# Performance work log

Hardware: AMD Instinct MI355X
Metric: run time of the kernel (lower is better)

Reference implementation:

```python
import jax, jax.numpy as jnp
import numpy as np

N_NODES = 100000
N_EDGES = 3200000
D_FEAT = 128
HIDDEN = 16
N_CLASSES = 8


def setup_inputs() -> dict:
    key = jax.random.key(0)
    k1, k2, k3, k4 = jax.random.split(key, 4)
    x = jax.random.normal(k1, (N_NODES, D_FEAT), dtype=jnp.float32)
    edge_index = jax.random.randint(k2, (2, N_EDGES), 0, N_NODES, dtype=jnp.int64)
    W1 = jax.random.normal(k3, (D_FEAT, HIDDEN), dtype=jnp.float32) * (1.0 / np.sqrt(D_FEAT))
    b1 = jnp.zeros((HIDDEN,), dtype=jnp.float32)
    W2 = jax.random.normal(k4, (HIDDEN, N_CLASSES), dtype=jnp.float32) * (1.0 / np.sqrt(HIDDEN))
    b2 = jnp.zeros((N_CLASSES,), dtype=jnp.float32)
    return {"x": x, "edge_index": edge_index, "W1": W1, "b1": b1, "W2": W2, "b2": b2}


def _gcn_conv(x, W, b, src, dst, deg_inv_sqrt, n_nodes):
    h = x @ W  # [N, F_out]
    norm = deg_inv_sqrt[src] * deg_inv_sqrt[dst]  # [E']
    msg = h[src] * norm[:, None]  # gather + scale
    out = jax.ops.segment_sum(msg, dst, num_segments=n_nodes)  # scatter-add
    return out + b


def _prep_edges(edge_index, n_nodes):
    # add self-loops (PyG GCNConv default) and compute symmetric norm degrees
    loop = jnp.arange(n_nodes, dtype=edge_index.dtype)
    src = jnp.concatenate([edge_index[0], loop])
    dst = jnp.concatenate([edge_index[1], loop])
    deg = jax.ops.segment_sum(jnp.ones_like(dst, dtype=jnp.float32), dst,
                              num_segments=n_nodes)
    deg_inv_sqrt = jnp.where(deg > 0, jax.lax.rsqrt(jnp.maximum(deg, 1.0)), 0.0)
    return src, dst, deg_inv_sqrt


def reference(x, edge_index, W1, b1, W2, b2):
    n_nodes = x.shape[0]
    src, dst, deg_inv_sqrt = _prep_edges(edge_index, n_nodes)
    h = jax.nn.relu(_gcn_conv(x, W1, b1, src, dst, deg_inv_sqrt, n_nodes))
    logits = _gcn_conv(h, W2, b2, src, dst, deg_inv_sqrt, n_nodes)
    return jax.nn.log_softmax(logits, axis=1)
```

## Files before the change

kernel.cpp:

```cpp
#include <hip/hip_runtime.h>

#define N_NODES 100000
#define N_EDGES 3200000
#define D_FEAT 128
#define HIDDEN 16
#define NCLS 8
#define NB_SCAN ((N_NODES + 255) / 256)


__global__ void k_deg_init(unsigned* __restrict__ deg) {
    int i = blockIdx.x * blockDim.x + threadIdx.x;
    if (i < N_NODES) deg[i] = 0u;
}

__global__ void k_deg_count(const int* __restrict__ dst, unsigned* __restrict__ deg) {
    int i = blockIdx.x * blockDim.x + threadIdx.x;
    if (i < N_EDGES) atomicAdd(&deg[dst[i]], 1u);
}

__global__ void k_dis(const unsigned* __restrict__ deg, float* __restrict__ dis) {
    int i = blockIdx.x * blockDim.x + threadIdx.x;
    if (i < N_NODES) dis[i] = rsqrtf((float)(deg[i] + 1u));
}

__global__ void k_scan1(const unsigned* __restrict__ deg, unsigned* __restrict__ rp,
                        unsigned* __restrict__ bsum) {
    __shared__ unsigned s[256];
    int tid = threadIdx.x;
    int i = blockIdx.x * 256 + tid;
    unsigned v = (i < N_NODES) ? deg[i] : 0u;
    s[tid] = v; __syncthreads();
    for (int off = 1; off < 256; off <<= 1) {
        unsigned t = (tid >= off) ? s[tid - off] : 0u;
        __syncthreads();
        s[tid] += t;
        __syncthreads();
    }
    if (i < N_NODES) rp[i] = s[tid] - v;
    if (tid == 255) bsum[blockIdx.x] = s[255];
}

__global__ void k_scan2(unsigned* __restrict__ bsum) {
    __shared__ unsigned s[512];
    int tid = threadIdx.x;
    unsigned v = (tid < NB_SCAN) ? bsum[tid] : 0u;
    s[tid] = v; __syncthreads();
    for (int off = 1; off < 512; off <<= 1) {
        unsigned t = (tid >= off) ? s[tid - off] : 0u;
        __syncthreads();
        s[tid] += t;
        __syncthreads();
    }
    bsum[tid] = s[tid] - v;
}

__global__ void k_scan3(unsigned* __restrict__ rp, const unsigned* __restrict__ bsum) {
    int i = blockIdx.x * blockDim.x + threadIdx.x;
    if (i < N_NODES) rp[i] += bsum[i >> 8];
}

__global__ void k_csr_fill(const int* __restrict__ src, const int* __restrict__ dst,
                           unsigned* __restrict__ rp, unsigned* __restrict__ csr) {
    int e = blockIdx.x * blockDim.x + threadIdx.x;
    if (e < N_EDGES) {
        unsigned p = atomicAdd(&rp[dst[e]], 1u);
        csr[p] = (unsigned)src[e];
    }
}

__global__ __launch_bounds__(256) void k_gemm1(const float* __restrict__ x,
                                               const float* __restrict__ W1,
                                               const float* __restrict__ dis,
                                               float* __restrict__ hd1) {
    __shared__ float sW[D_FEAT * HIDDEN];
    __shared__ float sx[64][132];
    int tid = threadIdx.x;
    for (int t = tid; t < D_FEAT * HIDDEN; t += 256) sW[t] = W1[t];

    int node0 = blockIdx.x * 64;
    #pragma unroll
    for (int it = 0; it < 8; ++it) {
        int lin = it * 256 + tid;
        int r   = lin >> 5;
        int c4  = lin & 31;
        int row = node0 + r;
        float4 v = make_float4(0.f, 0.f, 0.f, 0.f);
        if (row < N_NODES)
            v = *(const float4*)(x + (size_t)row * D_FEAT + c4 * 4);
        *(float4*)(&sx[r][c4 * 4]) = v;
    }
    __syncthreads();

    int lr   = tid >> 2;
    int node = node0 + lr;
    int f0   = (tid & 3) * 4;
    if (node >= N_NODES) return;

    float a0 = 0.f, a1 = 0.f, a2 = 0.f, a3 = 0.f;
    #pragma unroll
    for (int k = 0; k < D_FEAT; ++k) {
        float xv = sx[lr][k];
        a0 += xv * sW[k * HIDDEN + f0 + 0];
        a1 += xv * sW[k * HIDDEN + f0 + 1];
        a2 += xv * sW[k * HIDDEN + f0 + 2];
        a3 += xv * sW[k * HIDDEN + f0 + 3];
    }
    float s = dis[node];
    *(float4*)(hd1 + (size_t)node * HIDDEN + f0) = make_float4(a0 * s, a1 * s, a2 * s, a3 * s);
}

__global__ __launch_bounds__(256) void k_gather16_l2(
        const unsigned* __restrict__ rp, const unsigned* __restrict__ csr,
        const float* __restrict__ hd1, const float* __restrict__ dis,
        const float* __restrict__ b1, const float* __restrict__ W2,
        float* __restrict__ hd2) {
    __shared__ float sh[16][17];
    __shared__ float sW2[HIDDEN * NCLS];
    __shared__ float sb1[HIDDEN];
    int tid = threadIdx.x;
    if (tid < HIDDEN * NCLS) sW2[tid] = W2[tid];
    if (tid < HIDDEN)        sb1[tid] = b1[tid];

    int n = tid >> 4;
    int j = tid & 15;
    int node = blockIdx.x * 16 + n;

    unsigned start = (node == 0) ? 0u : rp[node - 1];
    unsigned end   = rp[node];
    float acc = hd1[(size_t)node * HIDDEN + j];
    for (unsigned e = start; e < end; ++e) {
        unsigned s = csr[e];
        acc += hd1[(size_t)s * HIDDEN + j];
    }
    float dv = dis[node];
    __syncthreads();
    float h = fmaxf(dv * acc + sb1[j], 0.f);
    sh[n][j] = h;
    __syncthreads();
    if (j < NCLS) {
        float o = 0.f;
        #pragma unroll
        for (int m = 0; m < HIDDEN; ++m) o += sh[n][m] * sW2[m * NCLS + j];
        hd2[(size_t)node * NCLS + j] = dv * o;
    }
}

__global__ __launch_bounds__(256) void k_gather8_final(
        const unsigned* __restrict__ rp, const unsigned* __restrict__ csr,
        const float* __restrict__ hd2, const float* __restrict__ dis,
        const float* __restrict__ b2, float* __restrict__ out) {
    int tid = threadIdx.x;
    int node = blockIdx.x * 32 + (tid >> 3);
    int j = tid & 7;

    unsigned start = (node == 0) ? 0u : rp[node - 1];
    unsigned end   = rp[node];
    float acc = hd2[(size_t)node * NCLS + j];
    for (unsigned e = start; e < end; ++e)
        acc += hd2[(size_t)csr[e] * NCLS + j];

    float l = dis[node] * acc + b2[j];
    float m = l;
    m = fmaxf(m, __shfl_xor(m, 1, 8));
    m = fmaxf(m, __shfl_xor(m, 2, 8));
    m = fmaxf(m, __shfl_xor(m, 4, 8));
    float ex = __expf(l - m);
    float ssum = ex;
    ssum += __shfl_xor(ssum, 1, 8);
    ssum += __shfl_xor(ssum, 2, 8);
    ssum += __shfl_xor(ssum, 4, 8);
    out[(size_t)node * NCLS + j] = l - (logf(ssum) + m);
}

extern "C" void kernel_launch(void* const* d_in, const int* in_sizes, int n_in,
                              void* d_out, int out_size, void* d_ws, size_t ws_size,
                              hipStream_t stream) {
    const float* x  = (const float*)d_in[0];
    const int*   ei = (const int*)d_in[1];
    const float* W1 = (const float*)d_in[2];
    const float* b1 = (const float*)d_in[3];
    const float* W2 = (const float*)d_in[4];
    const float* b2 = (const float*)d_in[5];
    float* out = (float*)d_out;

    const int* src = ei;
    const int* dst = ei + N_EDGES;

    unsigned* ws = (unsigned*)d_ws;
    const size_t N = N_NODES;
    unsigned* deg  = ws;
    float*    dis  = (float*)(ws + N);
    unsigned* rp   = ws + 2 * N;
    unsigned* bsum = ws + 3 * N;
    unsigned* csr  = ws + 3 * N + 512;
    float*    hd1  = (float*)(ws + 3 * N + 512 + N_EDGES);
    float*    hd2  = hd1 + 16 * N;

    const int TB = 256;
    int nb_nodes = (N_NODES + TB - 1) / TB;
    int nb_edges = (N_EDGES + TB - 1) / TB;

    k_deg_init<<<nb_nodes, TB, 0, stream>>>(deg);
    k_deg_count<<<nb_edges, TB, 0, stream>>>(dst, deg);
    k_dis<<<nb_nodes, TB, 0, stream>>>(deg, dis);

    k_scan1<<<NB_SCAN, 256, 0, stream>>>(deg, rp, bsum);
    k_scan2<<<1, 512, 0, stream>>>(bsum);
    k_scan3<<<nb_nodes, TB, 0, stream>>>(rp, bsum);
    k_csr_fill<<<nb_edges, TB, 0, stream>>>(src, dst, rp, csr);

    k_gemm1<<<(N_NODES + 63) / 64, TB, 0, stream>>>(x, W1, dis, hd1);

    k_gather16_l2<<<N_NODES / 16, TB, 0, stream>>>(rp, csr, hd1, dis, b1, W2, hd2);
    k_gather8_final<<<N_NODES / 32, TB, 0, stream>>>(rp, csr, hd2, dis, b2, out);
}
```

Before: 693.2 us.

## Replace per-node CSR with bucketed edge partition and shared-memory atomic aggregation

Drops the full per-node CSR build (global atomics for degree and fill) in favour of a coarse 256-bucket counting sort of edges by destination. Each edge is packed as src<<9 | local dst. Degrees and both aggregation layers are then computed per bucket with LDS atomics into a shared accumulator. This cuts global atomic contention and the node-level scan, but leaves only 256 blocks for the aggregation, adds LDS atomic contention, and turns each gather into an irregular read.

New measurement: 597.9 us. -13.8%, faster.

```diff
diff --git a/kernel.cpp b/kernel.cpp
--- a/kernel.cpp
+++ b/kernel.cpp
@@ -5,30 +5,36 @@
 #define D_FEAT 128
 #define HIDDEN 16
 #define NCLS 8
-#define NB_SCAN ((N_NODES + 255) / 256)
-
-
-__global__ void k_deg_init(unsigned* __restrict__ deg) {
-    int i = blockIdx.x * blockDim.x + threadIdx.x;
-    if (i < N_NODES) deg[i] = 0u;
-}
-
-__global__ void k_deg_count(const int* __restrict__ dst, unsigned* __restrict__ deg) {
-    int i = blockIdx.x * blockDim.x + threadIdx.x;
-    if (i < N_EDGES) atomicAdd(&deg[dst[i]], 1u);
-}
-
-__global__ void k_dis(const unsigned* __restrict__ deg, float* __restrict__ dis) {
-    int i = blockIdx.x * blockDim.x + threadIdx.x;
-    if (i < N_NODES) dis[i] = rsqrtf((float)(deg[i] + 1u));
-}
-
-__global__ void k_scan1(const unsigned* __restrict__ deg, unsigned* __restrict__ rp,
-                        unsigned* __restrict__ bsum) {
+
+#define NBKT 256
+#define BSZ  391
+#define CHUNK 8192
+#define NCHUNK 391
+#define TOTH (NBKT * NCHUNK)
+#define NBS1 (TOTH / 256)
+
+
+__global__ __launch_bounds__(256) void k_hist(const int* __restrict__ dst,
+                                              unsigned* __restrict__ hist) {
+    __shared__ unsigned h[NBKT];
+    int tid = threadIdx.x;
+    h[tid] = 0u;
+    __syncthreads();
+    int base = blockIdx.x * CHUNK;
+    #pragma unroll
+    for (int it = 0; it < CHUNK / 256; ++it) {
+        int e = base + it * 256 + tid;
+        if (e < N_EDGES) atomicAdd(&h[dst[e] / BSZ], 1u);
+    }
+    __syncthreads();
+    hist[(unsigned)tid * NCHUNK + blockIdx.x] = h[tid];
+}
+
+__global__ void k_scan1(unsigned* __restrict__ a, unsigned* __restrict__ bsum) {
     __shared__ unsigned s[256];
     int tid = threadIdx.x;
     int i = blockIdx.x * 256 + tid;
-    unsigned v = (i < N_NODES) ? deg[i] : 0u;
+    unsigned v = a[i];
     s[tid] = v; __syncthreads();
     for (int off = 1; off < 256; off <<= 1) {
         unsigned t = (tid >= off) ? s[tid - off] : 0u;
@@ -36,14 +42,14 @@
         s[tid] += t;
         __syncthreads();
     }
-    if (i < N_NODES) rp[i] = s[tid] - v;
+    a[i] = s[tid] - v;
     if (tid == 255) bsum[blockIdx.x] = s[255];
 }
 
 __global__ void k_scan2(unsigned* __restrict__ bsum) {
     __shared__ unsigned s[512];
     int tid = threadIdx.x;
-    unsigned v = (tid < NB_SCAN) ? bsum[tid] : 0u;
+    unsigned v = (tid < NBS1) ? bsum[tid] : 0u;
     s[tid] = v; __syncthreads();
     for (int off = 1; off < 512; off <<= 1) {
         unsigned t = (tid >= off) ? s[tid - off] : 0u;
@@ -54,18 +60,49 @@
     bsum[tid] = s[tid] - v;
 }
 
-__global__ void k_scan3(unsigned* __restrict__ rp, const unsigned* __restrict__ bsum) {
+__global__ void k_scan3(unsigned* __restrict__ a, const unsigned* __restrict__ bsum) {
     int i = blockIdx.x * blockDim.x + threadIdx.x;
-    if (i < N_NODES) rp[i] += bsum[i >> 8];
-}
-
-__global__ void k_csr_fill(const int* __restrict__ src, const int* __restrict__ dst,
-                           unsigned* __restrict__ rp, unsigned* __restrict__ csr) {
-    int e = blockIdx.x * blockDim.x + threadIdx.x;
-    if (e < N_EDGES) {
-        unsigned p = atomicAdd(&rp[dst[e]], 1u);
-        csr[p] = (unsigned)src[e];
-    }
+    a[i] += bsum[i >> 8];
+}
+
+__global__ __launch_bounds__(256) void k_fill(const int* __restrict__ src,
+                                              const int* __restrict__ dst,
+                                              const unsigned* __restrict__ hist,
+                                              unsigned* __restrict__ rec) {
+    __shared__ unsigned cur[NBKT];
+    int tid = threadIdx.x;
+    cur[tid] = hist[(unsigned)tid * NCHUNK + blockIdx.x];
+    __syncthreads();
+    int base = blockIdx.x * CHUNK;
+    #pragma unroll
+    for (int it = 0; it < CHUNK / 256; ++it) {
+        int e = base + it * 256 + tid;
+        if (e < N_EDGES) {
+            int d = dst[e];
+            int b = d / BSZ;
+            unsigned p = atomicAdd(&cur[b], 1u);
+            rec[p] = ((unsigned)src[e] << 9) | (unsigned)(d - b * BSZ);
+        }
+    }
+}
+
+__global__ __launch_bounds__(1024) void k_dis2(const unsigned* __restrict__ hist,
+                                               const unsigned* __restrict__ rec,
+                                               float* __restrict__ dis) {
+    __shared__ unsigned cnt[BSZ];
+    int tid = threadIdx.x;
+    int bkt = blockIdx.x;
+    int node0 = bkt * BSZ;
+    int nn = (node0 + BSZ <= N_NODES) ? BSZ : (N_NODES - node0);
+    for (int n = tid; n < nn; n += 1024) cnt[n] = 1u;
+    __syncthreads();
+    unsigned start = hist[(unsigned)bkt * NCHUNK];
+    unsigned end = (bkt == NBKT - 1) ? N_EDGES : hist[(unsigned)(bkt + 1) * NCHUNK];
+    for (unsigned e = start + tid; e < end; e += 1024)
+        atomicAdd(&cnt[rec[e] & 511u], 1u);
+    __syncthreads();
+    for (int n = tid; n < nn; n += 1024)
+        dis[node0 + n] = rsqrtf((float)cnt[n]);
 }
 
 __global__ __launch_bounds__(256) void k_gemm1(const float* __restrict__ x,
@@ -109,67 +146,103 @@
     *(float4*)(hd1 + (size_t)node * HIDDEN + f0) = make_float4(a0 * s, a1 * s, a2 * s, a3 * s);
 }
 
-__global__ __launch_bounds__(256) void k_gather16_l2(
-        const unsigned* __restrict__ rp, const unsigned* __restrict__ csr,
-        const float* __restrict__ hd1, const float* __restrict__ dis,
-        const float* __restrict__ b1, const float* __restrict__ W2,
-        float* __restrict__ hd2) {
-    __shared__ float sh[16][17];
+__global__ __launch_bounds__(1024) void k_aggB(const unsigned* __restrict__ hist,
+                                               const unsigned* __restrict__ rec,
+                                               const float* __restrict__ hd1,
+                                               const float* __restrict__ dis,
+                                               const float* __restrict__ b1,
+                                               const float* __restrict__ W2,
+                                               float* __restrict__ hd2) {
+    __shared__ float acc[BSZ][HIDDEN + 1];
     __shared__ float sW2[HIDDEN * NCLS];
     __shared__ float sb1[HIDDEN];
     int tid = threadIdx.x;
+    int bkt = blockIdx.x;
+    int node0 = bkt * BSZ;
+    int nn = (node0 + BSZ <= N_NODES) ? BSZ : (N_NODES - node0);
     if (tid < HIDDEN * NCLS) sW2[tid] = W2[tid];
     if (tid < HIDDEN)        sb1[tid] = b1[tid];
 
-    int n = tid >> 4;
-    int j = tid & 15;
-    int node = blockIdx.x * 16 + n;
-
-    unsigned start = (node == 0) ? 0u : rp[node - 1];
-    unsigned end   = rp[node];
-    float acc = hd1[(size_t)node * HIDDEN + j];
-    for (unsigned e = start; e < end; ++e) {
-        unsigned s = csr[e];
-        acc += hd1[(size_t)s * HIDDEN + j];
-    }
-    float dv = dis[node];
-    __syncthreads();
-    float h = fmaxf(dv * acc + sb1[j], 0.f);
-    sh[n][j] = h;
-    __syncthreads();
-    if (j < NCLS) {
-        float o = 0.f;
-        #pragma unroll
-        for (int m = 0; m < HIDDEN; ++m) o += sh[n][m] * sW2[m * NCLS + j];
-        hd2[(size_t)node * NCLS + j] = dv * o;
-    }
-}
-
-__global__ __launch_bounds__(256) void k_gather8_final(
-        const unsigned* __restrict__ rp, const unsigned* __restrict__ csr,
-        const float* __restrict__ hd2, const float* __restrict__ dis,
-        const float* __restrict__ b2, float* __restrict__ out) {
-    int tid = threadIdx.x;
-    int node = blockIdx.x * 32 + (tid >> 3);
-    int j = tid & 7;
-
-    unsigned start = (node == 0) ? 0u : rp[node - 1];
-    unsigned end   = rp[node];
-    float acc = hd2[(size_t)node * NCLS + j];
-    for (unsigned e = start; e < end; ++e)
-        acc += hd2[(size_t)csr[e] * NCLS + j];
-
-    float l = dis[node] * acc + b2[j];
-    float m = l;
-    m = fmaxf(m, __shfl_xor(m, 1, 8));
-    m = fmaxf(m, __shfl_xor(m, 2, 8));
-    m = fmaxf(m, __shfl_xor(m, 4, 8));
-    float ex = __expf(l - m);
-    float ssum = ex;
-    ssum += __shfl_xor(ssum, 1, 8);
-    ssum += __shfl_xor(ssum, 2, 8);
-    ssum += __shfl_xor(ssum, 4, 8);
-    out[(size_t)node * NCLS + j] = l - (logf(ssum) + m);
+    int j = tid & 15, rr = tid >> 4;
+    for (int r = rr; r < nn; r += 64)
+        acc[r][j] = hd1[(size_t)(node0 + r) * HIDDEN + j];
+    __syncthreads();
+
+    unsigned start = hist[(unsigned)bkt * NCHUNK];
+    unsigned end = (bkt == NBKT - 1) ? N_EDGES : hist[(unsigned)(bkt + 1) * NCHUNK];
+    for (unsigned e = start + rr; e < end; e += 64) {
+        unsigned r = rec[e];
+        unsigned s = r >> 9, dl = r & 511u;
+        float v = hd1[(size_t)s * HIDDEN + j];
+        atomicAdd(&acc[dl][j], v);
+    }
+    __syncthreads();
+
+    for (int n = tid; n < nn; n += 1024) {
+        int node = node0 + n;
+        float dv = dis[node];
+        float hbuf[HIDDEN];
+        #pragma unroll
+        for (int m = 0; m < HIDDEN; ++m)
+            hbuf[m] = fmaxf(dv * acc[n][m] + sb1[m], 0.f);
+        float o[NCLS];
+        #pragma unroll
+        for (int k = 0; k < NCLS; ++k) {
+            float t = 0.f;
+            #pragma unroll
+            for (int m = 0; m < HIDDEN; ++m) t += hbuf[m] * sW2[m * NCLS + k];
+            o[k] = dv * t;
+        }
+        float4* hp = (float4*)(hd2 + (size_t)node * NCLS);
+        hp[0] = make_float4(o[0], o[1], o[2], o[3]);
+        hp[1] = make_float4(o[4], o[5], o[6], o[7]);
+    }
+}
+
+__global__ __launch_bounds__(1024) void k_aggC(const unsigned* __restrict__ hist,
+                                               const unsigned* __restrict__ rec,
+                                               const float* __restrict__ hd2,
+                                               const float* __restrict__ dis,
+                                               const float* __restrict__ b2,
+                                               float* __restrict__ out) {
+    __shared__ float acc[BSZ][NCLS + 1];
+    int tid = threadIdx.x;
+    int bkt = blockIdx.x;
+    int node0 = bkt * BSZ;
+    int nn = (node0 + BSZ <= N_NODES) ? BSZ : (N_NODES - node0);
+
+    int j = tid & 7, rr = tid >> 3;
+    for (int r = rr; r < nn; r += 128)
+        acc[r][j] = hd2[(size_t)(node0 + r) * NCLS + j];
+    __syncthreads();
+
+    unsigned start = hist[(unsigned)bkt * NCHUNK];
+    unsigned end = (bkt == NBKT - 1) ? N_EDGES : hist[(unsigned)(bkt + 1) * NCHUNK];
+    for (unsigned e = start + rr; e < end; e += 128) {
+        unsigned r = rec[e];
+        unsigned s = r >> 9, dl = r & 511u;
+        atomicAdd(&acc[dl][j], hd2[(size_t)s * NCLS + j]);
+    }
+    __syncthreads();
+
+    for (int n = tid; n < nn; n += 1024) {
+        int node = node0 + n;
+        float dv = dis[node];
+        float l[NCLS];
+        float m = -1e30f;
+        #pragma unroll
+        for (int k = 0; k < NCLS; ++k) {
+            l[k] = dv * acc[n][k] + b2[k];
+            m = fmaxf(m, l[k]);
+        }
+        float ssum = 0.f;
+        #pragma unroll
+        for (int k = 0; k < NCLS; ++k) ssum += __expf(l[k] - m);
+        float lse = logf(ssum) + m;
+        float4* op = (float4*)(out + (size_t)node * NCLS);
+        op[0] = make_float4(l[0] - lse, l[1] - lse, l[2] - lse, l[3] - lse);
+        op[1] = make_float4(l[4] - lse, l[5] - lse, l[6] - lse, l[7] - lse);
+    }
 }
 
 extern "C" void kernel_launch(void* const* d_in, const int* in_sizes, int n_in,
@@ -188,29 +261,20 @@
 
     unsigned* ws = (unsigned*)d_ws;
     const size_t N = N_NODES;
-    unsigned* deg  = ws;
-    float*    dis  = (float*)(ws + N);
-    unsigned* rp   = ws + 2 * N;
-    unsigned* bsum = ws + 3 * N;
-    unsigned* csr  = ws + 3 * N + 512;
-    float*    hd1  = (float*)(ws + 3 * N + 512 + N_EDGES);
+    float*    dis  = (float*)ws;
+    unsigned* hist = ws + N;
+    unsigned* bsum = hist + TOTH;
+    unsigned* rec  = bsum + 512;
+    float*    hd1  = (float*)(rec + N_EDGES);
     float*    hd2  = hd1 + 16 * N;
 
-    const int TB = 256;
-    int nb_nodes = (N_NODES + TB - 1) / TB;
-    int nb_edges = (N_EDGES + TB - 1) / TB;
-
-    k_deg_init<<<nb_nodes, TB, 0, stream>>>(deg);
-    k_deg_count<<<nb_edges, TB, 0, stream>>>(dst, deg);
-    k_dis<<<nb_nodes, TB, 0, stream>>>(deg, dis);
-
-    k_scan1<<<NB_SCAN, 256, 0, stream>>>(deg, rp, bsum);
+    k_hist <<<NCHUNK, 256, 0, stream>>>(dst, hist);
+    k_scan1<<<NBS1, 256, 0, stream>>>(hist, bsum);
     k_scan2<<<1, 512, 0, stream>>>(bsum);
-    k_scan3<<<nb_nodes, TB, 0, stream>>>(rp, bsum);
-    k_csr_fill<<<nb_edges, TB, 0, stream>>>(src, dst, rp, csr);
-
-    k_gemm1<<<(N_NODES + 63) / 64, TB, 0, stream>>>(x, W1, dis, hd1);
-
-    k_gather16_l2<<<N_NODES / 16, TB, 0, stream>>>(rp, csr, hd1, dis, b1, W2, hd2);
-    k_gather8_final<<<N_NODES / 32, TB, 0, stream>>>(rp, csr, hd2, dis, b2, out);
-}
+    k_scan3<<<NBS1, 256, 0, stream>>>(hist, bsum);
+    k_fill <<<NCHUNK, 256, 0, stream>>>(src, dst, hist, rec);
+    k_dis2 <<<NBKT, 1024, 0, stream>>>(hist, rec, dis);
+    k_gemm1<<<(N_NODES + 63) / 64, 256, 0, stream>>>(x, W1, dis, hd1);
+    k_aggB <<<NBKT, 1024, 0, stream>>>(hist, rec, hd1, dis, b1, W2, hd2);
+    k_aggC <<<NBKT, 1024, 0, stream>>>(hist, rec, hd2, dis, b2, out);
+}
```
